# Kernel optimization log

Hardware: AMD Instinct MI355X
Metric: run time of the kernel (lower is better)

The kernel has to match this reference:

```python
import jax, jax.numpy as jnp
import numpy as np

N = 50000      # nodes
E = 800000     # edges
F_IN = 256     # num_n_feature
EMB = 128      # emb_size
GF = 32        # num_g_feature
G = 256        # graphs in batch
NEG_SLOPE = 0.2


def setup_inputs() -> dict:
    key = jax.random.key(0)
    ks = jax.random.split(key, 20)
    p = lambda i, shape: (jax.random.normal(ks[i], shape, jnp.float32) * 0.05)
    return {
        "x": jax.random.normal(ks[0], (N, F_IN), jnp.float32),
        "edges_idx": jax.random.randint(ks[1], (2, E), 0, N, dtype=jnp.int32),
        "batch_idx": jnp.sort(jax.random.randint(ks[2], (N,), 0, G, dtype=jnp.int32)),
        "g_features": jax.random.normal(ks[3], (G, GF), jnp.float32),
        # GATConv 1
        "W1": p(4, (F_IN, EMB)), "a1_src": p(5, (EMB,)), "a1_dst": p(6, (EMB,)), "b1": p(7, (EMB,)),
        # GATConv 2
        "W2": p(8, (EMB, EMB)), "a2_src": p(9, (EMB,)), "a2_dst": p(10, (EMB,)), "b2": p(11, (EMB,)),
        # lin_g
        "Wg": p(12, (GF, EMB)), "bg": p(13, (EMB,)),
        # out head: Linear(3*emb, 2)
        "Wo": p(14, (3 * EMB, 2)), "bo": p(15, (2,)),
    }


def gat_conv(x, src, dst, W, a_src, a_dst, b, n):
    """PyG GATConv, heads=1, with self-loops; attention dropout omitted (eval)."""
    h = x @ W                                  # [N, emb]
    loop = jnp.arange(n, dtype=src.dtype)
    src = jnp.concatenate([src, loop])         # add self loops
    dst = jnp.concatenate([dst, loop])
    e = jax.nn.leaky_relu((h @ a_src)[src] + (h @ a_dst)[dst], NEG_SLOPE)  # [E+N]
    # segment softmax over destination nodes
    m = jax.lax.stop_gradient(jax.ops.segment_max(e, dst, num_segments=n))
    m = jnp.where(jnp.isfinite(m), m, 0.0)
    p = jnp.exp(e - m[dst])
    den = jax.ops.segment_sum(p, dst, num_segments=n)
    alpha = p / den[dst]
    out = jax.ops.segment_sum(alpha[:, None] * h[src], dst, num_segments=n)
    return out + b


def reference(x, edges_idx, batch_idx, g_features,
              W1, a1_src, a1_dst, b1, W2, a2_src, a2_dst, b2,
              Wg, bg, Wo, bo):
    src, dst = edges_idx[0], edges_idx[1]
    h = gat_conv(x, src, dst, W1, a1_src, a1_dst, b1, N)
    h = gat_conv(h, src, dst, W2, a2_src, a2_dst, b2, N)
    # global mean / max pooling per graph
    counts = jax.ops.segment_sum(jnp.ones((N,), h.dtype), batch_idx, num_segments=G)
    mean = jax.ops.segment_sum(h, batch_idx, num_segments=G) / jnp.maximum(counts, 1.0)[:, None]
    mx = jax.ops.segment_max(h, batch_idx, num_segments=G)
    mx = jnp.where(jnp.isfinite(mx), mx, 0.0)
    g_ft = g_features @ Wg + bg
    flat = jnp.concatenate([mean, mx, g_ft], axis=1)   # [G, 3*emb]
    return jax.nn.log_softmax(flat @ Wo + bo, axis=-1)  # [G, 2]
```

## Files before the change

### kernel.cpp

```cpp
#include <hip/hip_runtime.h>
#include <hip/hip_bf16.h>

#define N_NODES 50000
#define N_EDGES 800000
#define FIN 256
#define EMB 128
#define NGRAPH 256
#define TOT_E (N_EDGES + N_NODES)
#define NP 98
#define RBLK 196
#define NB 391

typedef __bf16 bf16;
typedef __attribute__((ext_vector_type(8))) __bf16 bf16x8;
typedef __attribute__((ext_vector_type(4))) __bf16 bf16x4;
typedef __attribute__((ext_vector_type(2))) __bf16 bf16x2;
typedef __attribute__((ext_vector_type(4))) float f32x4;
typedef __attribute__((ext_vector_type(4))) int i32x4;

__global__ void transpose_kernel(const float* __restrict__ src, bf16* __restrict__ dst,
                                 int rows, int cols) {
    int t = blockIdx.x * 256 + threadIdx.x;
    if (t >= rows * cols) return;
    int c = t / rows, r = t - c * rows;
    dst[t] = (bf16)src[r * cols + c];
}

__global__ __launch_bounds__(256)
void hist_part_kernel(const int* __restrict__ e_dst, int* __restrict__ counts,
                      int* __restrict__ mat) {
    __shared__ int lh[NP];
    int t = threadIdx.x;
    for (int k = t; k < NP; k += 256) lh[k] = 0;
    __syncthreads();
    const int NQ = N_EDGES / 4;
    int base = blockIdx.x * 1024;
#pragma unroll
    for (int j = 0; j < 4; ++j) {
        int i = base + j * 256 + t;
        if (i < NQ) {
            i32x4 d4 = *(const i32x4*)(e_dst + 4 * i);
#pragma unroll
            for (int k = 0; k < 4; ++k) {
                atomicAdd(&counts[d4[k]], 1);
                atomicAdd(&lh[d4[k] >> 9], 1);
            }
        }
    }
    __syncthreads();
    for (int k = t; k < NP; k += 256) mat[k * RBLK + blockIdx.x] = lh[k];
}

__global__ __launch_bounds__(1024)
void scan_block_kernel(const int* __restrict__ counts, int* __restrict__ offsets,
                       int* __restrict__ blocksums) {
    __shared__ int lds[1024];
    int t = threadIdx.x;
    int idx = blockIdx.x * 1024 + t;
    int v = (idx < N_NODES) ? counts[idx] + 1 : 0;
    lds[t] = v;
    __syncthreads();
    for (int d = 1; d < 1024; d <<= 1) {
        int u = (t >= d) ? lds[t - d] : 0;
        __syncthreads();
        lds[t] += u;
        __syncthreads();
    }
    if (idx < N_NODES) offsets[idx] = lds[t] - v;
    if (t == 1023) blocksums[blockIdx.x] = lds[1023];
}

__global__ __launch_bounds__(1024)
void scan_fix_kernel(int* __restrict__ offsets, const int* __restrict__ blocksums,
                     int nblk, int* __restrict__ sorted) {
    __shared__ int sprefix;
    int t = threadIdx.x, b = blockIdx.x;
    if (t < 64) {
        int v = (t < b && t < nblk) ? blocksums[t] : 0;
#pragma unroll
        for (int mk = 32; mk >= 1; mk >>= 1) v += __shfl_xor(v, mk);
        if (t == 0) sprefix = v;
    }
    __syncthreads();
    int idx = b * 1024 + t;
    if (idx < N_NODES) {
        int off = offsets[idx] + sprefix;
        offsets[idx] = off;
        sorted[off] = idx;
    }
    if (idx == 0) offsets[N_NODES] = TOT_E;
}

__global__ __launch_bounds__(256)
void rowscan_kernel(int* __restrict__ mat, int* __restrict__ rowsum) {
    __shared__ int lds[256];
    int p = blockIdx.x, t = threadIdx.x;
    int v = (t < RBLK) ? mat[p * RBLK + t] : 0;
    lds[t] = v;
    __syncthreads();
    for (int d = 1; d < 256; d <<= 1) {
        int u = (t >= d) ? lds[t - d] : 0;
        __syncthreads();
        lds[t] += u;
        __syncthreads();
    }
    if (t < RBLK) mat[p * RBLK + t] = lds[t] - v;
    if (t == 255) rowsum[p] = lds[255];
}

__global__ __launch_bounds__(128)
void partbase_kernel(const int* __restrict__ rowsum, int* __restrict__ poff) {
    __shared__ int lds[128];
    int t = threadIdx.x;
    int v = (t < NP) ? rowsum[t] : 0;
    lds[t] = v;
    __syncthreads();
    for (int d = 1; d < 128; d <<= 1) {
        int u = (t >= d) ? lds[t - d] : 0;
        __syncthreads();
        lds[t] += u;
        __syncthreads();
    }
    if (t < NP) poff[t] = lds[t] - v;
    if (t == 0) poff[NP] = N_EDGES;
}

__global__ __launch_bounds__(256)
void radix_scatter_kernel(const int* __restrict__ e_src, const int* __restrict__ e_dst,
                          const int* __restrict__ mat, const int* __restrict__ poff,
                          unsigned* __restrict__ pairs) {
    __shared__ int cur[NP];
    int t = threadIdx.x;
    for (int k = t; k < NP; k += 256) cur[k] = poff[k] + mat[k * RBLK + blockIdx.x];
    __syncthreads();
    const int NQ = N_EDGES / 4;
    int base = blockIdx.x * 1024;
#pragma unroll
    for (int j = 0; j < 4; ++j) {
        int i = base + j * 256 + t;
        if (i < NQ) {
            i32x4 d4 = *(const i32x4*)(e_dst + 4 * i);
            i32x4 s4 = *(const i32x4*)(e_src + 4 * i);
#pragma unroll
            for (int k = 0; k < 4; ++k) {
                int d = d4[k];
                int pos = atomicAdd(&cur[d >> 9], 1);
                pairs[pos] = ((unsigned)d << 16) | (unsigned)s4[k];
            }
        }
    }
}

__global__ __launch_bounds__(1024)
void bucket_place_kernel(const int* __restrict__ poff, const int* __restrict__ offsets,
                         const unsigned* __restrict__ pairs, int* __restrict__ sorted) {
    int b = blockIdx.x;
    int t = threadIdx.x;
    int lo = b * 128;
    __shared__ int cur[128];
    if (t < 128 && lo + t < N_NODES) cur[t] = offsets[lo + t] + 1;
    __syncthreads();
    int p = b >> 2;
    int p0 = poff[p], p1 = poff[p + 1];
    unsigned blo = (unsigned)b;
    for (int i = p0 + t; i < p1; i += 1024) {
        unsigned v = pairs[i];
        unsigned d = v >> 16;
        if ((d >> 7) == blo) {
            int pos = atomicAdd(&cur[d & 127], 1);
            sorted[pos] = (int)(v & 0xFFFFu);
        }
    }
}

template<int K, typename AT>
__global__ __launch_bounds__(256)
void gemm_kernel(const AT* __restrict__ A, const bf16* __restrict__ WT,
                 bf16* __restrict__ C, int M,
                 const float* __restrict__ a_src, const float* __restrict__ a_dst,
                 float* __restrict__ s_src, float* __restrict__ s_dst) {
    __shared__ __align__(16) bf16 As[64][64];
    __shared__ __align__(16) bf16 Bs[128][64];
    int tid = threadIdx.x;
    int wave = tid >> 6, lane = tid & 63;
    int m0 = blockIdx.x * 64;

    f32x4 acc[8];
#pragma unroll
    for (int i = 0; i < 8; ++i) acc[i] = (f32x4){0.f, 0.f, 0.f, 0.f};

    for (int k0 = 0; k0 < K; k0 += 64) {
        if constexpr (sizeof(AT) == 4) {
#pragma unroll
            for (int it = 0; it < 4; ++it) {
                int task = tid + it * 256;
                int row = task >> 4, seg4 = task & 15;
                int gr = m0 + row;
                float4 f = make_float4(0.f, 0.f, 0.f, 0.f);
                if (gr < M) f = *(const float4*)((const float*)A + (size_t)gr * K + k0 + seg4 * 4);
                bf16x4 b4 = (bf16x4){(bf16)f.x, (bf16)f.y, (bf16)f.z, (bf16)f.w};
                int slot = seg4 >> 1, half8 = seg4 & 1;
                int ss = slot ^ (row & 7);
                *(bf16x4*)(&As[row][ss * 8 + half8 * 4]) = b4;
            }
        } else {
#pragma unroll
            for (int it = 0; it < 2; ++it) {
                int task = tid + it * 256;
                int row = task >> 3, slot = task & 7;
                int gr = m0 + row;
                uint4 v = make_uint4(0u, 0u, 0u, 0u);
                if (gr < M) v = *(const uint4*)((const bf16*)A + (size_t)gr * K + k0 + slot * 8);
                int ss = slot ^ (row & 7);
                *(uint4*)(&As[row][ss * 8]) = v;
            }
        }
#pragma unroll
        for (int it = 0; it < 4; ++it) {
            int task = tid + it * 256;
            int col = task >> 3, slot = task & 7;
            uint4 v = *(const uint4*)(WT + (size_t)col * K + k0 + slot * 8);
            int ss = slot ^ (col & 7);
            *(uint4*)(&Bs[col][ss * 8]) = v;
        }
        __syncthreads();
        int r = wave * 16 + (lane & 15);
        int kk = lane >> 4;
        bf16x8 af0 = *(const bf16x8*)(&As[r][((kk) ^ (r & 7)) * 8]);
        bf16x8 af1 = *(const bf16x8*)(&As[r][((4 + kk) ^ (r & 7)) * 8]);
#pragma unroll
        for (int n = 0; n < 8; ++n) {
            int c = n * 16 + (lane & 15);
            bf16x8 b0 = *(const bf16x8*)(&Bs[c][((kk) ^ (c & 7)) * 8]);
            bf16x8 b1 = *(const bf16x8*)(&Bs[c][((4 + kk) ^ (c & 7)) * 8]);
            acc[n] = __builtin_amdgcn_mfma_f32_16x16x32_bf16(af0, b0, acc[n], 0, 0, 0);
            acc[n] = __builtin_amdgcn_mfma_f32_16x16x32_bf16(af1, b1, acc[n], 0, 0, 0);
        }
        __syncthreads();
    }
    int rbase = m0 + wave * 16 + ((lane >> 4) << 2);
    int cbase = lane & 15;
#pragma unroll
    for (int n = 0; n < 8; ++n) {
#pragma unroll
        for (int r = 0; r < 4; ++r) {
            int row = rbase + r;
            if (row < M) C[(size_t)row * 128 + n * 16 + cbase] = (bf16)acc[n][r];
        }
    }
    float a_s[8], a_d[8];
#pragma unroll
    for (int n = 0; n < 8; ++n) {
        a_s[n] = a_src[n * 16 + cbase];
        a_d[n] = a_dst[n * 16 + cbase];
    }
#pragma unroll
    for (int r = 0; r < 4; ++r) {
        float ps = 0.f, pd = 0.f;
#pragma unroll
        for (int n = 0; n < 8; ++n) {
            ps += acc[n][r] * a_s[n];
            pd += acc[n][r] * a_d[n];
        }
#pragma unroll
        for (int mk = 8; mk >= 1; mk >>= 1) {
            ps += __shfl_xor(ps, mk);
            pd += __shfl_xor(pd, mk);
        }
        int row = rbase + r;
        if (cbase == 0 && row < M) { s_src[row] = ps; s_dst[row] = pd; }
    }
}

template<typename OUT_T>
__global__ __launch_bounds__(256)
void agg_kernel(const int* __restrict__ offsets, const int* __restrict__ sorted_src,
                const float* __restrict__ s_src, const float* __restrict__ s_dst,
                const bf16* __restrict__ h, const float* __restrict__ bias,
                OUT_T* __restrict__ out) {
    int tid = threadIdx.x;
    int wave = tid >> 6, lane = tid & 63;
    int gl = lane & 15;
    int gbase = lane & 48;
    int d = blockIdx.x * 16 + wave * 4 + (lane >> 4);
    if (d >= N_NODES) return;
    int r0 = offsets[d];
    int deg = offsets[d + 1] - r0;
    float sd = s_dst[d];

    int sv0 = 0, sv1 = 0;
    float ev0 = -INFINITY, ev1 = -INFINITY;
    if (gl < deg) {
        sv0 = sorted_src[r0 + gl];
        float e = s_src[sv0] + sd;
        ev0 = (e > 0.f) ? e : 0.2f * e;
    }
    if (16 + gl < deg) {
        sv1 = sorted_src[r0 + 16 + gl];
        float e = s_src[sv1] + sd;
        ev1 = (e > 0.f) ? e : 0.2f * e;
    }
    float m = fmaxf(ev0, ev1);
    for (int i = 32 + gl; i < deg; i += 16) {
        int s = sorted_src[r0 + i];
        float e = s_src[s] + sd;
        e = (e > 0.f) ? e : 0.2f * e;
        m = fmaxf(m, e);
    }
#pragma unroll
    for (int mk = 8; mk >= 1; mk >>= 1) m = fmaxf(m, __shfl_xor(m, mk));

    float pv0 = (gl < deg) ? __expf(ev0 - m) : 0.f;
    float pv1 = (16 + gl < deg) ? __expf(ev1 - m) : 0.f;
    float den = pv0 + pv1;
    for (int i = 32 + gl; i < deg; i += 16) {
        int s = sorted_src[r0 + i];
        float e = s_src[s] + sd;
        e = (e > 0.f) ? e : 0.2f * e;
        den += __expf(e - m);
    }
#pragma unroll
    for (int mk = 8; mk >= 1; mk >>= 1) den += __shfl_xor(den, mk);

    float acc[8];
#pragma unroll
    for (int k = 0; k < 8; ++k) acc[k] = 0.f;

    int jm = (deg < 32) ? deg : 32;
#pragma unroll 4
    for (int j = 0; j < jm; ++j) {
        int src_lane = gbase + (j & 15);
        int s = __shfl((j < 16) ? sv0 : sv1, src_lane);
        float p = __shfl((j < 16) ? pv0 : pv1, src_lane);
        bf16x8 hv = *(const bf16x8*)(h + (size_t)s * 128 + gl * 8);
#pragma unroll
        for (int k = 0; k < 8; ++k) acc[k] += p * (float)hv[k];
    }
    for (int i = 32; i < deg; ++i) {
        int s = sorted_src[r0 + i];
        float e = s_src[s] + sd;
        e = (e > 0.f) ? e : 0.2f * e;
        float p = __expf(e - m);
        bf16x8 hv = *(const bf16x8*)(h + (size_t)s * 128 + gl * 8);
#pragma unroll
        for (int k = 0; k < 8; ++k) acc[k] += p * (float)hv[k];
    }

    float inv = 1.f / den;
    float4 bv0 = *(const float4*)(bias + gl * 8);
    float4 bv1 = *(const float4*)(bias + gl * 8 + 4);
    float o[8] = {acc[0] * inv + bv0.x, acc[1] * inv + bv0.y,
                  acc[2] * inv + bv0.z, acc[3] * inv + bv0.w,
                  acc[4] * inv + bv1.x, acc[5] * inv + bv1.y,
                  acc[6] * inv + bv1.z, acc[7] * inv + bv1.w};
    if constexpr (sizeof(OUT_T) == 2) {
        bf16x8 ov;
#pragma unroll
        for (int k = 0; k < 8; ++k) ov[k] = (bf16)o[k];
        *(bf16x8*)((bf16*)out + (size_t)d * 128 + gl * 8) = ov;
    } else {
        float* op = (float*)out + (size_t)d * 128 + gl * 8;
        *(float4*)op       = (float4){o[0], o[1], o[2], o[3]};
        *(float4*)(op + 4) = (float4){o[4], o[5], o[6], o[7]};
    }
}

__global__ __launch_bounds__(256)
void pool_kernel(const bf16* __restrict__ out2, const int* __restrict__ batch_idx,
                 float* __restrict__ mean, float* __restrict__ mx) {
    int g = blockIdx.x;
    int j = threadIdx.x & 127;
    int grp = threadIdx.x >> 7;
    int lo = 0, hi = N_NODES;
    while (lo < hi) { int mid = (lo + hi) >> 1; if (batch_idx[mid] < g) lo = mid + 1; else hi = mid; }
    int start = lo;
    hi = N_NODES;
    while (lo < hi) { int mid = (lo + hi) >> 1; if (batch_idx[mid] < g + 1) lo = mid + 1; else hi = mid; }
    int end = lo;

    float s = 0.f, mmax = -INFINITY;
    for (int r = start + grp; r < end; r += 2) {
        float v = (float)out2[(size_t)r * 128 + j];
        s += v;
        mmax = fmaxf(mmax, v);
    }
    __shared__ float ls[2][128], lm[2][128];
    ls[grp][j] = s; lm[grp][j] = mmax;
    __syncthreads();
    if (grp == 0) {
        int cnt = end - start;
        float sum = ls[0][j] + ls[1][j];
        float mv = fmaxf(lm[0][j], lm[1][j]);
        mean[g * 128 + j] = sum / fmaxf((float)cnt, 1.f);
        mx[g * 128 + j] = (cnt > 0) ? mv : 0.f;
    }
}

__global__ __launch_bounds__(128)
void head_kernel(const float* __restrict__ mean, const float* __restrict__ mx,
                 const float* __restrict__ gfeat, const float* __restrict__ Wg,
                 const float* __restrict__ bg, const float* __restrict__ Wo,
                 const float* __restrict__ bo, float* __restrict__ out) {
    int g = blockIdx.x;
    int j = threadIdx.x;
    float gft = bg[j];
#pragma unroll
    for (int k = 0; k < 32; ++k)
        gft += gfeat[g * 32 + k] * Wg[k * 128 + j];
    float mj = mean[g * 128 + j], xj = mx[g * 128 + j];
    float p0 = mj * Wo[j * 2 + 0] + xj * Wo[(128 + j) * 2 + 0] + gft * Wo[(256 + j) * 2 + 0];
    float p1 = mj * Wo[j * 2 + 1] + xj * Wo[(128 + j) * 2 + 1] + gft * Wo[(256 + j) * 2 + 1];
#pragma unroll
    for (int m = 32; m >= 1; m >>= 1) { p0 += __shfl_xor(p0, m); p1 += __shfl_xor(p1, m); }
    __shared__ float l0s[2], l1s[2];
    int wv = j >> 6;
    if ((j & 63) == 0) { l0s[wv] = p0; l1s[wv] = p1; }
    __syncthreads();
    if (j == 0) {
        float l0 = l0s[0] + l0s[1] + bo[0];
        float l1 = l1s[0] + l1s[1] + bo[1];
        float mm = fmaxf(l0, l1);
        float lse = mm + logf(__expf(l0 - mm) + __expf(l1 - mm));
        out[g * 2 + 0] = l0 - lse;
        out[g * 2 + 1] = l1 - lse;
    }
}

extern "C" void kernel_launch(void* const* d_in, const int* in_sizes, int n_in,
                              void* d_out, int out_size, void* d_ws, size_t ws_size,
                              hipStream_t stream) {
    const float* x     = (const float*)d_in[0];
    const int*   edges = (const int*)d_in[1];
    const int*   batch = (const int*)d_in[2];
    const float* gfeat = (const float*)d_in[3];
    const float* W1    = (const float*)d_in[4];
    const float* a1s   = (const float*)d_in[5];
    const float* a1d   = (const float*)d_in[6];
    const float* b1    = (const float*)d_in[7];
    const float* W2    = (const float*)d_in[8];
    const float* a2s   = (const float*)d_in[9];
    const float* a2d   = (const float*)d_in[10];
    const float* b2    = (const float*)d_in[11];
    const float* Wg    = (const float*)d_in[12];
    const float* bg    = (const float*)d_in[13];
    const float* Wo    = (const float*)d_in[14];
    const float* bo    = (const float*)d_in[15];

    char* ws = (char*)d_ws;
    bf16*     WT1       = (bf16*)(ws + 0);
    bf16*     WT2       = (bf16*)(ws + 65536);
    float*    s_src     = (float*)(ws + 98304);
    float*    s_dst     = (float*)(ws + 299008);
    int*      counts    = (int*)(ws + 499712);
    int*      blocksums = (int*)(ws + 700416);
    int*      mat       = (int*)(ws + 700672);
    int*      rowsum    = (int*)(ws + 777536);
    int*      poff      = (int*)(ws + 777984);
    int*      offsets   = (int*)(ws + 778432);
    int*      sorted    = (int*)(ws + 979136);
    bf16*     h         = (bf16*)(ws + 4502528);
    bf16*     out1      = (bf16*)(ws + 17302528);
    bf16*     out2      = (bf16*)(ws + 30102528);
    unsigned* pairs     = (unsigned*)(ws + 43002528);
    float*    pmean     = (float*)(ws + 55702528);
    float*    pmax      = (float*)(ws + 55833600);

    const int* e_src = edges;
    const int* e_dst = edges + N_EDGES;

    transpose_kernel<<<(FIN * EMB + 255) / 256, 256, 0, stream>>>(W1, WT1, FIN, EMB);
    transpose_kernel<<<(EMB * EMB + 255) / 256, 256, 0, stream>>>(W2, WT2, EMB, EMB);

    hipMemsetAsync(counts, 0, N_NODES * sizeof(int), stream);
    hist_part_kernel<<<RBLK, 256, 0, stream>>>(e_dst, counts, mat);
    int nblk = (N_NODES + 1023) / 1024;
    scan_block_kernel<<<nblk, 1024, 0, stream>>>(counts, offsets, blocksums);
    scan_fix_kernel<<<nblk, 1024, 0, stream>>>(offsets, blocksums, nblk, sorted);
    rowscan_kernel<<<NP, 256, 0, stream>>>(mat, rowsum);
    partbase_kernel<<<1, 128, 0, stream>>>(rowsum, poff);
    radix_scatter_kernel<<<RBLK, 256, 0, stream>>>(e_src, e_dst, mat, poff, pairs);
    bucket_place_kernel<<<NB, 1024, 0, stream>>>(poff, offsets, pairs, sorted);

    int gemm_blocks = (N_NODES + 63) / 64;
    int agg_blocks = (N_NODES + 15) / 16;

    gemm_kernel<FIN, float><<<gemm_blocks, 256, 0, stream>>>(x, WT1, h, N_NODES,
                                                             a1s, a1d, s_src, s_dst);
    agg_kernel<bf16><<<agg_blocks, 256, 0, stream>>>(offsets, sorted, s_src, s_dst, h, b1, out1);

    gemm_kernel<EMB, bf16><<<gemm_blocks, 256, 0, stream>>>(out1, WT2, h, N_NODES,
                                                            a2s, a2d, s_src, s_dst);
    agg_kernel<bf16><<<agg_blocks, 256, 0, stream>>>(offsets, sorted, s_src, s_dst, h, b2, out2);

    pool_kernel<<<NGRAPH, 256, 0, stream>>>(out2, batch, pmean, pmax);
    head_kernel<<<NGRAPH, 128, 0, stream>>>(pmean, pmax, gfeat, Wg, bg, Wo, bo, (float*)d_out);
}
```

Before: 213.4 us.

## Halve GEMM row tile, split columns across waves, fuse weight transposes

The GEMM row tile drops from 64 to 32 rows, and the 4 waves are now arranged 2x2 over rows and column halves. Blocks double to about 1563, giving more parallelism across the CUs, and the attention score reductions are combined through shared-memory atomics. In exchange, each block reloads the full 128-column weight tile for half as many rows, which doubles total weight traffic and adds extra barriers. The two weight transpose launches are merged into one kernel, and the aggregation gather loop unroll rises from 4 to 8.

Result: no change. 213.9 us (+0.2%).

```diff
diff --git a/kernel.cpp b/kernel.cpp
--- a/kernel.cpp
+++ b/kernel.cpp
@@ -18,12 +18,17 @@
 typedef __attribute__((ext_vector_type(4))) float f32x4;
 typedef __attribute__((ext_vector_type(4))) int i32x4;
 
-__global__ void transpose_kernel(const float* __restrict__ src, bf16* __restrict__ dst,
-                                 int rows, int cols) {
+__global__ void transpose2_kernel(const float* __restrict__ W1, bf16* __restrict__ WT1,
+                                  const float* __restrict__ W2, bf16* __restrict__ WT2) {
     int t = blockIdx.x * 256 + threadIdx.x;
-    if (t >= rows * cols) return;
-    int c = t / rows, r = t - c * rows;
-    dst[t] = (bf16)src[r * cols + c];
+    if (t < FIN * EMB) {
+        int c = t / FIN, r = t - c * FIN;
+        WT1[t] = (bf16)W1[r * EMB + c];
+    } else if (t < FIN * EMB + EMB * EMB) {
+        int u = t - FIN * EMB;
+        int c = u / EMB, r = u - c * EMB;
+        WT2[u] = (bf16)W2[r * EMB + c];
+    }
 }
 
 __global__ __launch_bounds__(256)
@@ -179,20 +184,22 @@
                  bf16* __restrict__ C, int M,
                  const float* __restrict__ a_src, const float* __restrict__ a_dst,
                  float* __restrict__ s_src, float* __restrict__ s_dst) {
-    __shared__ __align__(16) bf16 As[64][64];
+    __shared__ __align__(16) bf16 As[32][64];
     __shared__ __align__(16) bf16 Bs[128][64];
+    __shared__ float sbuf[2][32];
     int tid = threadIdx.x;
     int wave = tid >> 6, lane = tid & 63;
-    int m0 = blockIdx.x * 64;
-
-    f32x4 acc[8];
-#pragma unroll
-    for (int i = 0; i < 8; ++i) acc[i] = (f32x4){0.f, 0.f, 0.f, 0.f};
+    int rowHalf = wave & 1, colHalf = wave >> 1;
+    int m0 = blockIdx.x * 32;
+
+    f32x4 acc[4];
+#pragma unroll
+    for (int i = 0; i < 4; ++i) acc[i] = (f32x4){0.f, 0.f, 0.f, 0.f};
 
     for (int k0 = 0; k0 < K; k0 += 64) {
         if constexpr (sizeof(AT) == 4) {
 #pragma unroll
-            for (int it = 0; it < 4; ++it) {
+            for (int it = 0; it < 2; ++it) {
                 int task = tid + it * 256;
                 int row = task >> 4, seg4 = task & 15;
                 int gr = m0 + row;
@@ -204,16 +211,12 @@
                 *(bf16x4*)(&As[row][ss * 8 + half8 * 4]) = b4;
             }
         } else {
-#pragma unroll
-            for (int it = 0; it < 2; ++it) {
-                int task = tid + it * 256;
-                int row = task >> 3, slot = task & 7;
-                int gr = m0 + row;
-                uint4 v = make_uint4(0u, 0u, 0u, 0u);
-                if (gr < M) v = *(const uint4*)((const bf16*)A + (size_t)gr * K + k0 + slot * 8);
-                int ss = slot ^ (row & 7);
-                *(uint4*)(&As[row][ss * 8]) = v;
-            }
+            int row = tid >> 3, slot = tid & 7;
+            int gr = m0 + row;
+            uint4 v = make_uint4(0u, 0u, 0u, 0u);
+            if (gr < M) v = *(const uint4*)((const bf16*)A + (size_t)gr * K + k0 + slot * 8);
+            int ss = slot ^ (row & 7);
+            *(uint4*)(&As[row][ss * 8]) = v;
         }
 #pragma unroll
         for (int it = 0; it < 4; ++it) {
@@ -224,51 +227,62 @@
             *(uint4*)(&Bs[col][ss * 8]) = v;
         }
         __syncthreads();
-        int r = wave * 16 + (lane & 15);
-        int kk = lane >> 4;
-        bf16x8 af0 = *(const bf16x8*)(&As[r][((kk) ^ (r & 7)) * 8]);
-        bf16x8 af1 = *(const bf16x8*)(&As[r][((4 + kk) ^ (r & 7)) * 8]);
-#pragma unroll
-        for (int n = 0; n < 8; ++n) {
-            int c = n * 16 + (lane & 15);
-            bf16x8 b0 = *(const bf16x8*)(&Bs[c][((kk) ^ (c & 7)) * 8]);
-            bf16x8 b1 = *(const bf16x8*)(&Bs[c][((4 + kk) ^ (c & 7)) * 8]);
+        int tr = rowHalf * 16 + (lane & 15);
+        int kseg = lane >> 4;
+        bf16x8 af0 = *(const bf16x8*)(&As[tr][((kseg) ^ (tr & 7)) * 8]);
+        bf16x8 af1 = *(const bf16x8*)(&As[tr][((4 + kseg) ^ (tr & 7)) * 8]);
+#pragma unroll
+        for (int n = 0; n < 4; ++n) {
+            int c = colHalf * 64 + n * 16 + (lane & 15);
+            bf16x8 b0 = *(const bf16x8*)(&Bs[c][((kseg) ^ (c & 7)) * 8]);
+            bf16x8 b1 = *(const bf16x8*)(&Bs[c][((4 + kseg) ^ (c & 7)) * 8]);
             acc[n] = __builtin_amdgcn_mfma_f32_16x16x32_bf16(af0, b0, acc[n], 0, 0, 0);
             acc[n] = __builtin_amdgcn_mfma_f32_16x16x32_bf16(af1, b1, acc[n], 0, 0, 0);
         }
         __syncthreads();
     }
-    int rbase = m0 + wave * 16 + ((lane >> 4) << 2);
-    int cbase = lane & 15;
-#pragma unroll
-    for (int n = 0; n < 8; ++n) {
-#pragma unroll
-        for (int r = 0; r < 4; ++r) {
-            int row = rbase + r;
-            if (row < M) C[(size_t)row * 128 + n * 16 + cbase] = (bf16)acc[n][r];
-        }
-    }
-    float a_s[8], a_d[8];
-#pragma unroll
-    for (int n = 0; n < 8; ++n) {
-        a_s[n] = a_src[n * 16 + cbase];
-        a_d[n] = a_dst[n * 16 + cbase];
-    }
-#pragma unroll
-    for (int r = 0; r < 4; ++r) {
+    int rbase = m0 + rowHalf * 16 + ((lane >> 4) << 2);
+    int cb = lane & 15;
+#pragma unroll
+    for (int n = 0; n < 4; ++n) {
+        int col = colHalf * 64 + n * 16 + cb;
+#pragma unroll
+        for (int rr = 0; rr < 4; ++rr) {
+            int row = rbase + rr;
+            if (row < M) C[(size_t)row * 128 + col] = (bf16)acc[n][rr];
+        }
+    }
+    if (tid < 64) sbuf[tid >> 5][tid & 31] = 0.f;
+    __syncthreads();
+    float a_s[4], a_d[4];
+#pragma unroll
+    for (int n = 0; n < 4; ++n) {
+        a_s[n] = a_src[colHalf * 64 + n * 16 + cb];
+        a_d[n] = a_dst[colHalf * 64 + n * 16 + cb];
+    }
+#pragma unroll
+    for (int rr = 0; rr < 4; ++rr) {
         float ps = 0.f, pd = 0.f;
 #pragma unroll
-        for (int n = 0; n < 8; ++n) {
-            ps += acc[n][r] * a_s[n];
-            pd += acc[n][r] * a_d[n];
+        for (int n = 0; n < 4; ++n) {
+            ps += acc[n][rr] * a_s[n];
+            pd += acc[n][rr] * a_d[n];
         }
 #pragma unroll
         for (int mk = 8; mk >= 1; mk >>= 1) {
             ps += __shfl_xor(ps, mk);
             pd += __shfl_xor(pd, mk);
         }
-        int row = rbase + r;
-        if (cbase == 0 && row < M) { s_src[row] = ps; s_dst[row] = pd; }
+        if (cb == 0) {
+            int tr16 = rowHalf * 16 + (lane >> 4) * 4 + rr;
+            atomicAdd(&sbuf[0][tr16], ps);
+            atomicAdd(&sbuf[1][tr16], pd);
+        }
+    }
+    __syncthreads();
+    if (tid < 32 && m0 + tid < M) {
+        s_src[m0 + tid] = sbuf[0][tid];
+        s_dst[m0 + tid] = sbuf[1][tid];
     }
 }
 
@@ -327,7 +341,7 @@
     for (int k = 0; k < 8; ++k) acc[k] = 0.f;
 
     int jm = (deg < 32) ? deg : 32;
-#pragma unroll 4
+#pragma unroll 8
     for (int j = 0; j < jm; ++j) {
         int src_lane = gbase + (j & 15);
         int s = __shfl((j < 16) ? sv0 : sv1, src_lane);
@@ -468,8 +482,7 @@
     const int* e_src = edges;
     const int* e_dst = edges + N_EDGES;
 
-    transpose_kernel<<<(FIN * EMB + 255) / 256, 256, 0, stream>>>(W1, WT1, FIN, EMB);
-    transpose_kernel<<<(EMB * EMB + 255) / 256, 256, 0, stream>>>(W2, WT2, EMB, EMB);
+    transpose2_kernel<<<(FIN * EMB + EMB * EMB + 255) / 256, 256, 0, stream>>>(W1, WT1, W2, WT2);
 
     hipMemsetAsync(counts, 0, N_NODES * sizeof(int), stream);
     hist_part_kernel<<<RBLK, 256, 0, stream>>>(e_dst, counts, mat);
@@ -481,7 +494,7 @@
     radix_scatter_kernel<<<RBLK, 256, 0, stream>>>(e_src, e_dst, mat, poff, pairs);
     bucket_place_kernel<<<NB, 1024, 0, stream>>>(poff, offsets, pairs, sorted);
 
-    int gemm_blocks = (N_NODES + 63) / 64;
+    int gemm_blocks = (N_NODES + 31) / 32;
     int agg_blocks = (N_NODES + 15) / 16;
 
     gemm_kernel<FIN, float><<<gemm_blocks, 256, 0, stream>>>(x, WT1, h, N_NODES,
```
